# Optimization experiments

Measured on AMD Instinct MI355X. Metric: run time of the kernel, lower is better.

The kernel has to match this reference:

```python
import jax, jax.numpy as jnp
import numpy as np

NEG_FILL = -10000.0  # matches masked_fill_(mask, -10000.0)


def setup_inputs() -> dict:
    key0 = jax.random.key(0)
    kq, kk, kv, km = jax.random.split(key0, 4)
    B, H, S, D = 2, 16, 2048, 64
    query = jax.random.normal(kq, (B, H, S, D), dtype=jnp.float32)
    key = jax.random.normal(kk, (B, H, S, D), dtype=jnp.float32)
    value = jax.random.normal(kv, (B, H, S, D), dtype=jnp.float32)
    # key-padding mask [B, S]; True = position is masked out
    mask = jax.random.randint(km, (B, S), 0, 2).astype(jnp.bool_)
    return {"query": query, "key": key, "value": value, "mask": mask}


def reference(query, key, value, mask):
    # scaled dot-product attention: [B,H,S,D] x [B,H,S,D] -> [B,H,S,S]
    scale = 1.0 / jnp.sqrt(jnp.asarray(query.shape[-1], query.dtype))
    scores = jnp.einsum('bhqd,bhkd->bhqk', query, key) * scale
    # mask [B,S] -> broadcast over heads and query positions as [B,1,1,S]
    scores = jnp.where(mask[:, None, None, :], jnp.asarray(NEG_FILL, scores.dtype), scores)
    attn = jax.nn.softmax(scores, axis=-1)
    # dropout probs are 0 (eval-mode identity)
    out = jnp.einsum('bhqk,bhkd->bhqd', attn, value)
    return out
```

## Files before the change

### kernel.cpp

```cpp
#include <hip/hip_runtime.h>
#include <hip/hip_bf16.h>
#include <stdint.h>

namespace {

constexpr int Bb = 2;
constexpr int Hh = 16;
constexpr int Ss = 2048;
constexpr int Dd = 64;
constexpr int KT = 64;
constexpr int NT = Ss / KT;
constexpr int TILE_BYTES = KT * Dd * 2;
constexpr int BH_BYTES = NT * TILE_BYTES;
constexpr size_t KPRE_BYTES = (size_t)Bb * Hh * Ss * Dd * 2;
constexpr size_t VPRE_OFF = KPRE_BYTES;
constexpr size_t MASK_OFF = 2 * KPRE_BYTES;
constexpr size_t WS_NEED = MASK_OFF + (size_t)Bb * NT * 8;
constexpr int NIT = 16;
constexpr int IT_BYTES = 2 * TILE_BYTES;

typedef __bf16 bf16x8 __attribute__((ext_vector_type(8)));
typedef float floatx4 __attribute__((ext_vector_type(4)));

typedef __attribute__((address_space(1))) const unsigned int guint;
typedef __attribute__((address_space(3))) unsigned int luint;

__device__ __forceinline__ void g2lds16(const void* g, void* l) {
  __builtin_amdgcn_global_load_lds((guint*)g, (luint*)l, 16, 0, 0);
}

__global__ __launch_bounds__(256) void preprocess3(
    const float* __restrict__ K, const float* __restrict__ V,
    const int* __restrict__ mask, uint8_t* __restrict__ ws)
{
  const int tid = threadIdx.x;
  const int kt = blockIdx.x;
  const int bh = blockIdx.y;

  if (blockIdx.z == 0) {
    const int c = tid & 7;
#pragma unroll
    for (int half = 0; half < 2; ++half) {
      const int row = (tid >> 3) + half * 32;
      const float4* src = (const float4*)(K + ((size_t)bh * 2048 + kt * 64 + row) * 64 + c * 8);
      const float4 a = src[0], b2 = src[1];
      bf16x8 pk;
      pk[0] = (__bf16)a.x;  pk[1] = (__bf16)a.y;  pk[2] = (__bf16)a.z;  pk[3] = (__bf16)a.w;
      pk[4] = (__bf16)b2.x; pk[5] = (__bf16)b2.y; pk[6] = (__bf16)b2.z; pk[7] = (__bf16)b2.w;
      uint8_t* dst = ws + (size_t)bh * BH_BYTES + kt * TILE_BYTES + row * 128 + ((c ^ (row & 7)) << 4);
      *(bf16x8*)dst = pk;
    }
    if (bh == 0 && kt < 16) {
      const int i = kt * 256 + tid;
      const int bb = i >> 11, key = i & 2047;
      const unsigned long long bal = __ballot(mask[bb * 2048 + key] != 0);
      if ((key & 63) == 0)
        ((unsigned long long*)(ws + MASK_OFF))[bb * NT + (key >> 6)] = bal;
    }
    return;
  }

  __shared__ float Vsh[64 * 68];
#pragma unroll
  for (int i = 0; i < 4; ++i) {
    const int vt = tid + 256 * i;
    const int row = vt >> 4, c4 = vt & 15;
    const float4 v4 = *(const float4*)(V + ((size_t)bh * 2048 + kt * 64 + row) * 64 + c4 * 4);
    *(float4*)&Vsh[row * 68 + c4 * 4] = v4;
  }
  __syncthreads();
  {
    const int c16 = tid & 7;
    const int s2 = c16 & 1, q = c16 >> 1;
    const int k0 = 32 * s2 + 4 * q;
#pragma unroll
    for (int half = 0; half < 2; ++half) {
      const int d = (tid >> 3) + half * 32;
      bf16x8 pv;
#pragma unroll
      for (int j = 0; j < 4; ++j) {
        pv[j]     = (__bf16)Vsh[(k0 + j) * 68 + d];
        pv[4 + j] = (__bf16)Vsh[(k0 + 16 + j) * 68 + d];
      }
      uint8_t* dst = ws + VPRE_OFF + (size_t)bh * BH_BYTES + kt * TILE_BYTES + d * 128 + ((c16 ^ (d & 7)) << 4);
      *(bf16x8*)dst = pv;
    }
  }
}

#define NEGM (-14426.950408889634f)

__global__ __launch_bounds__(256, 2) void attn_fused6(
    const float* __restrict__ Q, const uint8_t* __restrict__ ws,
    float* __restrict__ Out)
{
  const int tid  = threadIdx.x;
  const int wave = tid >> 6;
  const int lane = tid & 63;
  const int ln   = lane & 15;
  const int quad = lane >> 4;

  const int bh   = blockIdx.x;
  const int qblk = blockIdx.y;
  const int b    = bh >> 4;

  const float* Qb = Q + (size_t)bh * Ss * Dd;
  float*       Ob = Out + (size_t)bh * Ss * Dd;
  const uint8_t* Kpre = ws + (size_t)bh * BH_BYTES;
  const uint8_t* Vpre = ws + VPRE_OFF + (size_t)bh * BH_BYTES;
  const unsigned long long* Mbits = (const unsigned long long*)(ws + MASK_OFF) + b * NT;

  __shared__ __align__(16) __bf16 Klds[2][128 * Dd];
  __shared__ __align__(16) __bf16 Vlds[2][128 * Dd];

  const int q0A = qblk * 128 + wave * 32;
  const int q0B = q0A + 16;

  const float QS = 0.125f * 1.44269504088896340736f;
  bf16x8 aqA0, aqA1, aqB0, aqB1;
  {
    const float* qpA = Qb + (size_t)(q0A + ln) * Dd + quad * 8;
    const float* qpB = Qb + (size_t)(q0B + ln) * Dd + quad * 8;
#pragma unroll
    for (int j = 0; j < 8; ++j) {
      aqA0[j] = (__bf16)(qpA[j] * QS);
      aqA1[j] = (__bf16)(qpA[32 + j] * QS);
      aqB0[j] = (__bf16)(qpB[j] * QS);
      aqB1[j] = (__bf16)(qpB[32 + j] * QS);
    }
  }

  floatx4 oA[4], oB[4];
  floatx4 laccA = (floatx4){0.f, 0.f, 0.f, 0.f};
  floatx4 laccB = (floatx4){0.f, 0.f, 0.f, 0.f};
#pragma unroll
  for (int nd = 0; nd < 4; ++nd) {
    oA[nd] = (floatx4){0.f, 0.f, 0.f, 0.f};
    oB[nd] = (floatx4){0.f, 0.f, 0.f, 0.f};
  }

  const int swz0 = (quad ^ (ln & 7)) << 4;
  const int swz1 = ((quad + 4) ^ (ln & 7)) << 4;
  const int soff = wave * 4096 + lane * 16;

#pragma unroll
  for (int i = 0; i < 4; ++i) {
    g2lds16(Kpre + soff + i * 1024, (uint8_t*)Klds[0] + soff + i * 1024);
    g2lds16(Vpre + soff + i * 1024, (uint8_t*)Vlds[0] + soff + i * 1024);
  }

  for (int kt2 = 0; kt2 < NIT; ++kt2) {
    const int cur = kt2 & 1;
    __syncthreads();

    if (kt2 + 1 < NIT) {
      const uint8_t* kg = Kpre + (kt2 + 1) * IT_BYTES;
      const uint8_t* vg = Vpre + (kt2 + 1) * IT_BYTES;
      uint8_t* kl = (uint8_t*)Klds[cur ^ 1];
      uint8_t* vl = (uint8_t*)Vlds[cur ^ 1];
#pragma unroll
      for (int i = 0; i < 4; ++i) {
        g2lds16(kg + soff + i * 1024, kl + soff + i * 1024);
        g2lds16(vg + soff + i * 1024, vl + soff + i * 1024);
      }
    }

    const unsigned long long mb0 = Mbits[2 * kt2];
    const unsigned long long mb1 = Mbits[2 * kt2 + 1];
    floatx4 biasC[8];
#pragma unroll
    for (int sub = 0; sub < 8; ++sub) {
      const unsigned long long mbx = (sub & 4) ? mb1 : mb0;
      const uint32_t bits = (uint32_t)(mbx >> ((sub & 3) * 16 + quad * 4));
#pragma unroll
      for (int r = 0; r < 4; ++r)
        biasC[sub][r] = ((bits >> r) & 1) ? NEGM : 0.f;
    }

    floatx4 sA[8], sB[8];
#pragma unroll
    for (int sub = 0; sub < 8; ++sub) {
      const uint8_t* krow = (const uint8_t*)Klds[cur] + (sub >> 2) * 8192 + ((sub & 3) * 16 + ln) * 128;
      const bf16x8 bk0 = *(const bf16x8*)(krow + swz0);
      const bf16x8 bk1 = *(const bf16x8*)(krow + swz1);
      floatx4 cA = biasC[sub];
      cA = __builtin_amdgcn_mfma_f32_16x16x32_bf16(bk0, aqA0, cA, 0, 0, 0);
      cA = __builtin_amdgcn_mfma_f32_16x16x32_bf16(bk1, aqA1, cA, 0, 0, 0);
      sA[sub] = cA;
      floatx4 cB = biasC[sub];
      cB = __builtin_amdgcn_mfma_f32_16x16x32_bf16(bk0, aqB0, cB, 0, 0, 0);
      cB = __builtin_amdgcn_mfma_f32_16x16x32_bf16(bk1, aqB1, cB, 0, 0, 0);
      sB[sub] = cB;
    }

    bf16x8 bpA[4], bpB[4];
#pragma unroll
    for (int sub = 0; sub < 8; ++sub) {
      const int pair = sub >> 1, u = sub & 1;
#pragma unroll
      for (int r = 0; r < 4; ++r) {
        const float pA = __builtin_amdgcn_exp2f(sA[sub][r]);
        const float pB = __builtin_amdgcn_exp2f(sB[sub][r]);
        laccA[r] += pA;
        laccB[r] += pB;
        bpA[pair][u * 4 + r] = (__bf16)pA;
        bpB[pair][u * 4 + r] = (__bf16)pB;
      }
    }

#pragma unroll
    for (int nd = 0; nd < 4; ++nd) {
#pragma unroll
      for (int T = 0; T < 2; ++T) {
        const uint8_t* vrow = (const uint8_t*)Vlds[cur] + T * 8192 + (nd * 16 + ln) * 128;
#pragma unroll
        for (int s2 = 0; s2 < 2; ++s2) {
          const bf16x8 w = *(const bf16x8*)(vrow + (((quad * 2 + s2) ^ (ln & 7)) << 4));
          const int pair = T * 2 + s2;
          oA[nd] = __builtin_amdgcn_mfma_f32_16x16x32_bf16(w, bpA[pair], oA[nd], 0, 0, 0);
          oB[nd] = __builtin_amdgcn_mfma_f32_16x16x32_bf16(w, bpB[pair], oB[nd], 0, 0, 0);
        }
      }
    }
  }

  float lA = (laccA[0] + laccA[1]) + (laccA[2] + laccA[3]);
  float lB = (laccB[0] + laccB[1]) + (laccB[2] + laccB[3]);
  lA += __shfl_xor(lA, 16); lA += __shfl_xor(lA, 32);
  lB += __shfl_xor(lB, 16); lB += __shfl_xor(lB, 32);
  const float iA = 1.0f / lA, iB = 1.0f / lB;
#pragma unroll
  for (int nd = 0; nd < 4; ++nd) {
    float4 wv;
    wv.x = oA[nd][0] * iA; wv.y = oA[nd][1] * iA;
    wv.z = oA[nd][2] * iA; wv.w = oA[nd][3] * iA;
    *(float4*)(Ob + (size_t)(q0A + ln) * Dd + nd * 16 + quad * 4) = wv;
    wv.x = oB[nd][0] * iB; wv.y = oB[nd][1] * iB;
    wv.z = oB[nd][2] * iB; wv.w = oB[nd][3] * iB;
    *(float4*)(Ob + (size_t)(q0B + ln) * Dd + nd * 16 + quad * 4) = wv;
  }
}

}

extern "C" void kernel_launch(void* const* d_in, const int* in_sizes, int n_in,
                              void* d_out, int out_size, void* d_ws, size_t ws_size,
                              hipStream_t stream) {
  const float* Q   = (const float*)d_in[0];
  const float* K   = (const float*)d_in[1];
  const float* V   = (const float*)d_in[2];
  const int*  mask = (const int*)d_in[3];
  float* Out = (float*)d_out;

  preprocess3<<<dim3(32, 32, 2), 256, 0, stream>>>(K, V, mask, (uint8_t*)d_ws);
  attn_fused6<<<dim3(Bb * Hh, Ss / 128), 256, 0, stream>>>(Q, (const uint8_t*)d_ws, Out);
  (void)ws_size; (void)in_sizes; (void)n_in; (void)out_size;
}
```

Baseline: 136.0 us.

## Software-pipeline K/V LDS fragment loads with QK, exp and PV MFMA per sub-tile pair

Restructures the inner tile loop into four stages, each covering a pair of 16-key sub-tiles. The next pair's K and V fragments are prefetched from LDS into double-buffered registers while the current pair runs QK MFMA, exp2 and PV MFMA. This interleaves LDS reads with matrix work instead of running three separate phases, and it raises wave priority with s_setprio during the loop. The extra live fragment registers could pressure occupancy at launch_bounds(256,2).

```diff
diff --git a/kernel.cpp b/kernel.cpp
--- a/kernel.cpp
+++ b/kernel.cpp
@@ -89,8 +89,9 @@
 }
 
 #define NEGM (-14426.950408889634f)
-
-__global__ __launch_bounds__(256, 2) void attn_fused6(
+#define MFMA16 __builtin_amdgcn_mfma_f32_16x16x32_bf16
+
+__global__ __launch_bounds__(256, 2) void attn_fused7(
     const float* __restrict__ Q, const uint8_t* __restrict__ ws,
     float* __restrict__ Out)
 {
@@ -167,61 +168,83 @@
 
     const unsigned long long mb0 = Mbits[2 * kt2];
     const unsigned long long mb1 = Mbits[2 * kt2 + 1];
-    floatx4 biasC[8];
-#pragma unroll
-    for (int sub = 0; sub < 8; ++sub) {
-      const unsigned long long mbx = (sub & 4) ? mb1 : mb0;
-      const uint32_t bits = (uint32_t)(mbx >> ((sub & 3) * 16 + quad * 4));
-#pragma unroll
-      for (int r = 0; r < 4; ++r)
-        biasC[sub][r] = ((bits >> r) & 1) ? NEGM : 0.f;
-    }
-
-    floatx4 sA[8], sB[8];
-#pragma unroll
-    for (int sub = 0; sub < 8; ++sub) {
-      const uint8_t* krow = (const uint8_t*)Klds[cur] + (sub >> 2) * 8192 + ((sub & 3) * 16 + ln) * 128;
-      const bf16x8 bk0 = *(const bf16x8*)(krow + swz0);
-      const bf16x8 bk1 = *(const bf16x8*)(krow + swz1);
-      floatx4 cA = biasC[sub];
-      cA = __builtin_amdgcn_mfma_f32_16x16x32_bf16(bk0, aqA0, cA, 0, 0, 0);
-      cA = __builtin_amdgcn_mfma_f32_16x16x32_bf16(bk1, aqA1, cA, 0, 0, 0);
-      sA[sub] = cA;
-      floatx4 cB = biasC[sub];
-      cB = __builtin_amdgcn_mfma_f32_16x16x32_bf16(bk0, aqB0, cB, 0, 0, 0);
-      cB = __builtin_amdgcn_mfma_f32_16x16x32_bf16(bk1, aqB1, cB, 0, 0, 0);
-      sB[sub] = cB;
-    }
-
-    bf16x8 bpA[4], bpB[4];
-#pragma unroll
-    for (int sub = 0; sub < 8; ++sub) {
-      const int pair = sub >> 1, u = sub & 1;
+
+    const uint8_t* Kb = (const uint8_t*)Klds[cur];
+    const uint8_t* Vb = (const uint8_t*)Vlds[cur];
+
+    auto loadK = [&](int sub, bf16x8& b0, bf16x8& b1) {
+      const uint8_t* krow = Kb + (sub >> 2) * 8192 + ((sub & 3) * 16 + ln) * 128;
+      b0 = *(const bf16x8*)(krow + swz0);
+      b1 = *(const bf16x8*)(krow + swz1);
+    };
+    auto loadV = [&](int p, bf16x8* w) {
+      const int T = p >> 1, s2 = p & 1;
+#pragma unroll
+      for (int nd = 0; nd < 4; ++nd) {
+        const uint8_t* vrow = Vb + T * 8192 + (nd * 16 + ln) * 128;
+        w[nd] = *(const bf16x8*)(vrow + (((quad * 2 + s2) ^ (ln & 7)) << 4));
+      }
+    };
+
+    __builtin_amdgcn_s_setprio(1);
+
+    bf16x8 kf0[2][2], kf1[2][2];
+    bf16x8 vf[2][4];
+    loadK(0, kf0[0][0], kf1[0][0]);
+    loadK(1, kf0[0][1], kf1[0][1]);
+    loadV(0, vf[0]);
+
+#pragma unroll
+    for (int p = 0; p < 4; ++p) {
+      const int cb = p & 1, nb = cb ^ 1;
+
+      if (p < 3) {
+        loadK(2 * p + 2, kf0[nb][0], kf1[nb][0]);
+        loadK(2 * p + 3, kf0[nb][1], kf1[nb][1]);
+        loadV(p + 1, vf[nb]);
+      }
+
+      const unsigned long long mbx = (p & 2) ? mb1 : mb0;
+      const uint32_t bits0 = (uint32_t)(mbx >> ((((2 * p) & 3) * 16) + quad * 4));
+      const uint32_t bits1 = (uint32_t)(mbx >> ((((2 * p + 1) & 3) * 16) + quad * 4));
+      floatx4 sA0, sA1, sB0, sB1;
 #pragma unroll
       for (int r = 0; r < 4; ++r) {
-        const float pA = __builtin_amdgcn_exp2f(sA[sub][r]);
-        const float pB = __builtin_amdgcn_exp2f(sB[sub][r]);
-        laccA[r] += pA;
-        laccB[r] += pB;
-        bpA[pair][u * 4 + r] = (__bf16)pA;
-        bpB[pair][u * 4 + r] = (__bf16)pB;
-      }
-    }
-
-#pragma unroll
-    for (int nd = 0; nd < 4; ++nd) {
-#pragma unroll
-      for (int T = 0; T < 2; ++T) {
-        const uint8_t* vrow = (const uint8_t*)Vlds[cur] + T * 8192 + (nd * 16 + ln) * 128;
-#pragma unroll
-        for (int s2 = 0; s2 < 2; ++s2) {
-          const bf16x8 w = *(const bf16x8*)(vrow + (((quad * 2 + s2) ^ (ln & 7)) << 4));
-          const int pair = T * 2 + s2;
-          oA[nd] = __builtin_amdgcn_mfma_f32_16x16x32_bf16(w, bpA[pair], oA[nd], 0, 0, 0);
-          oB[nd] = __builtin_amdgcn_mfma_f32_16x16x32_bf16(w, bpB[pair], oB[nd], 0, 0, 0);
-        }
-      }
-    }
+        const float b0v = ((bits0 >> r) & 1) ? NEGM : 0.f;
+        const float b1v = ((bits1 >> r) & 1) ? NEGM : 0.f;
+        sA0[r] = b0v; sB0[r] = b0v;
+        sA1[r] = b1v; sB1[r] = b1v;
+      }
+
+      sA0 = MFMA16(kf0[cb][0], aqA0, sA0, 0, 0, 0);
+      sA0 = MFMA16(kf1[cb][0], aqA1, sA0, 0, 0, 0);
+      sB0 = MFMA16(kf0[cb][0], aqB0, sB0, 0, 0, 0);
+      sB0 = MFMA16(kf1[cb][0], aqB1, sB0, 0, 0, 0);
+      sA1 = MFMA16(kf0[cb][1], aqA0, sA1, 0, 0, 0);
+      sA1 = MFMA16(kf1[cb][1], aqA1, sA1, 0, 0, 0);
+      sB1 = MFMA16(kf0[cb][1], aqB0, sB1, 0, 0, 0);
+      sB1 = MFMA16(kf1[cb][1], aqB1, sB1, 0, 0, 0);
+
+      bf16x8 bpA, bpB;
+#pragma unroll
+      for (int r = 0; r < 4; ++r) {
+        const float pA0 = __builtin_amdgcn_exp2f(sA0[r]);
+        const float pA1 = __builtin_amdgcn_exp2f(sA1[r]);
+        const float pB0 = __builtin_amdgcn_exp2f(sB0[r]);
+        const float pB1 = __builtin_amdgcn_exp2f(sB1[r]);
+        laccA[r] += pA0 + pA1;
+        laccB[r] += pB0 + pB1;
+        bpA[r] = (__bf16)pA0; bpA[4 + r] = (__bf16)pA1;
+        bpB[r] = (__bf16)pB0; bpB[4 + r] = (__bf16)pB1;
+      }
+
+#pragma unroll
+      for (int nd = 0; nd < 4; ++nd) {
+        oA[nd] = MFMA16(vf[cb][nd], bpA, oA[nd], 0, 0, 0);
+        oB[nd] = MFMA16(vf[cb][nd], bpB, oB[nd], 0, 0, 0);
+      }
+    }
+    __builtin_amdgcn_s_setprio(0);
   }
 
   float lA = (laccA[0] + laccA[1]) + (laccA[2] + laccA[3]);
@@ -253,6 +276,6 @@
   float* Out = (float*)d_out;
 
   preprocess3<<<dim3(32, 32, 2), 256, 0, stream>>>(K, V, mask, (uint8_t*)d_ws);
-  attn_fused6<<<dim3(Bb * Hh, Ss / 128), 256, 0, stream>>>(Q, (const uint8_t*)d_ws, Out);
+  attn_fused7<<<dim3(Bb * Hh, Ss / 128), 256, 0, stream>>>(Q, (const uint8_t*)d_ws, Out);
   (void)ws_size; (void)in_sizes; (void)n_in; (void)out_size;
 }
```

Result: no change. 135.3 us (-0.5%).
